# Kernel tuning notes

Hardware: AMD Instinct MI355X
Metric: run time of the kernel (lower is better)

The kernel has to match this reference:

```python
import jax, jax.numpy as jnp
import numpy as np

N = 50000   # nodes
E = 800000  # edges (avg degree 16)
G = 64      # graphs in batch
H = 4       # attention heads
D = 128     # hidden dim per head (= hidden_dim)
V = 128     # embedding vocab (input_dim)
NEG_SLOPE = 0.2

def setup_inputs() -> dict:
    key = jax.random.key(0)
    ks = jax.random.split(key, 12)
    s = 0.05
    return {
        "feats": jax.random.randint(ks[0], (N,), 0, V),
        "src": jax.random.randint(ks[1], (E,), 0, N),
        "dst": jax.random.randint(ks[2], (E,), 0, N),
        "graph_ids": jnp.sort(jax.random.randint(ks[3], (N,), 0, G)),
        "emb": jax.random.normal(ks[4], (V, D)) * s,
        "W1": jax.random.normal(ks[5], (D, H * D)) * s,
        "b1": jax.random.normal(ks[6], (H * D,)) * s,
        "a1": jax.random.normal(ks[7], (H, D)) * s,
        "W2": jax.random.normal(ks[8], (D, H * D)) * s,
        "b2": jax.random.normal(ks[9], (H * D,)) * s,
        "a2": jax.random.normal(ks[10], (H, D)) * s,
        "Wreg": jax.random.normal(ks[11], (1, D)) * s,
    }

def gatv2_layer(x, W, b, a, src, dst):
    # shared-weight GATv2: h = Wx + b, split into heads -> [N,H,D]
    h = (x @ W + b).reshape(-1, H, D)
    hs = h[src]                      # [E,H,D] source feats per edge
    hd = h[dst]                      # [E,H,D] dest feats per edge
    e = jax.nn.leaky_relu(hs + hd, NEG_SLOPE)
    logits = jnp.einsum('ehd,hd->eh', e, a)          # [E,H]
    # edge softmax over incoming edges of each dst node
    m = jax.ops.segment_max(logits, dst, num_segments=N)
    m = jnp.where(jnp.isfinite(m), m, 0.0)           # empty segments -> 0 (unused)
    ex = jnp.exp(logits - m[dst])
    denom = jax.ops.segment_sum(ex, dst, num_segments=N)
    alpha = ex / denom[dst]                          # [E,H]
    rst = jax.ops.segment_sum(alpha[:, :, None] * hs, dst, num_segments=N)  # [N,H,D]
    return rst.mean(axis=1)          # .mean(dim=1) over heads -> [N,D]

def reference(feats, src, dst, graph_ids, emb, W1, b1, a1, W2, b2, a2, Wreg):
    x = emb[feats]                                   # embedding lookup [N,D]
    x = gatv2_layer(x, W1, b1, a1, src, dst)         # layer 1 (dropout=0)
    x = gatv2_layer(x, W2, b2, a2, src, dst)         # layer 2
    pooled = jax.ops.segment_sum(x, graph_ids, num_segments=G)  # SumPooling [G,D]
    return pooled @ Wreg.T                           # Linear bias=False -> [G,1]
```

## Files before the change

### kernel.cpp

```cpp
#include <hip/hip_runtime.h>
#include <hip/hip_bf16.h>

#define N_NODES 50000
#define N_EDGES 800000
#define G_GRAPHS 64
#define H_HEADS 4
#define D_DIM 128
#define HD 512
#define V_VOCAB 128
#define NEG_SLOPE 0.2f

typedef float f32x2v __attribute__((ext_vector_type(2)));
typedef float f32x4 __attribute__((ext_vector_type(4)));
typedef short s16x8 __attribute__((ext_vector_type(8)));
typedef _Float16 h16x2 __attribute__((ext_vector_type(2)));

static __device__ __forceinline__ unsigned short f2b(float f) {
    union { float f; unsigned int i; } x; x.f = f;
    unsigned int r = x.i + 0x7fffu + ((x.i >> 16) & 1u);
    return (unsigned short)(r >> 16);
}
static __device__ __forceinline__ h16x2 u2h2(unsigned int u) {
    union { unsigned int u; h16x2 h; } c; c.u = u; return c.h;
}
static __device__ __forceinline__ unsigned int h22u(h16x2 h) {
    union { unsigned int u; h16x2 h; } c; c.h = h; return c.u;
}
static __device__ __forceinline__ h16x2 packf2(float lo, float hi) {
    union { __fp16 __attribute__((ext_vector_type(2))) p; h16x2 h; } c;
    c.p = __builtin_amdgcn_cvt_pkrtz(lo, hi);
    return c.h;
}

#if __has_builtin(__builtin_amdgcn_cvt_scalef32_pk_f16_fp8)
static __device__ __forceinline__ void fp8x4_to_h16(unsigned int u, h16x2& h0, h16x2& h1) {
    auto r0 = __builtin_amdgcn_cvt_scalef32_pk_f16_fp8((int)u, 1.0f, false);
    auto r1 = __builtin_amdgcn_cvt_scalef32_pk_f16_fp8((int)u, 1.0f, true);
    union { decltype(r0) p; h16x2 h; } c0, c1;
    c0.p = r0; c1.p = r1;
    h0 = c0.h; h1 = c1.h;
}
#else
static __device__ __forceinline__ void fp8x4_to_h16(unsigned int u, h16x2& h0, h16x2& h1) {
    f32x2v lo = __builtin_amdgcn_cvt_pk_f32_fp8(u, false);
    f32x2v hi = __builtin_amdgcn_cvt_pk_f32_fp8(u, true);
    h0 = packf2(lo.x, lo.y);
    h1 = packf2(hi.x, hi.y);
}
#endif

template<int CTRL>
static __device__ __forceinline__ float dpp_add(float v) {
    union { float f; int i; } a, b;
    a.f = v;
    b.i = __builtin_amdgcn_mov_dpp(a.i, CTRL, 0xF, 0xF, true);
    return v + b.f;
}
static __device__ __forceinline__ float row16_sum(float p) {
    p = dpp_add<0xB1>(p);
    p = dpp_add<0x4E>(p);
    p = dpp_add<0x141>(p);
    p = dpp_add<0x140>(p);
    return p;
}

#define MEGA_M1_BLOCKS   256
#define MEGA_WSZ_BLOCKS  256
#define MEGA_HIST_BLOCKS ((N_EDGES + 255) / 256)
__global__ void __launch_bounds__(256) mega_kernel(const float* __restrict__ emb,
                                                   const float* __restrict__ W1,
                                                   float* __restrict__ M1,
                                                   const float* __restrict__ W2,
                                                   unsigned short* __restrict__ Wb,
                                                   const int* __restrict__ dst,
                                                   int* __restrict__ counts,
                                                   float* __restrict__ pool) {
    int b = blockIdx.x;
    if (b < MEGA_M1_BLOCKS) {
        int idx = b * 256 + threadIdx.x;
        int v = idx >> 9, c = idx & 511;
        float acc = 0.f;
        for (int k = 0; k < 128; k++)
            acc += emb[v * 128 + k] * W1[k * 512 + c];
        M1[idx] = acc;
    } else if (b < MEGA_M1_BLOCKS + MEGA_WSZ_BLOCKS) {
        int idx = (b - MEGA_M1_BLOCKS) * 256 + threadIdx.x;
        int j = idx & 7, c = (idx >> 3) & 511, qq = idx >> 12;
        Wb[idx] = f2b(W2[(qq * 8 + j) * 512 + c]);
    } else {
        int hb = b - MEGA_M1_BLOCKS - MEGA_WSZ_BLOCKS;
        if (hb == 0 && threadIdx.x < G_GRAPHS) pool[threadIdx.x] = 0.f;
        int i = hb * 256 + threadIdx.x;
        if (i < N_EDGES) atomicAdd(&counts[dst[i]], 1);
    }
}

__global__ void __launch_bounds__(256) scanf_kernel(const int* __restrict__ counts,
                                                    int* __restrict__ offsets,
                                                    int* __restrict__ cursor,
                                                    int* __restrict__ bsum,
                                                    int* __restrict__ flag) {
    __shared__ int buf[256];
    __shared__ int sbase;
    int t = threadIdx.x, b = blockIdx.x;
    int i0 = (b * 256 + t) * 4;
    int v[4], c[4], s = 0;
    #pragma unroll
    for (int j = 0; j < 4; j++) {
        int idx = i0 + j;
        v[j] = (idx < N_NODES) ? counts[idx] : 0;
        s += v[j];
        c[j] = s;
    }
    buf[t] = s;
    __syncthreads();
    for (int off = 1; off < 256; off <<= 1) {
        int add = (t >= off) ? buf[t - off] : 0;
        __syncthreads();
        buf[t] += add;
        __syncthreads();
    }
    int ebase = (t > 0) ? buf[t - 1] : 0;
    if (t == 0) {
        bsum[b] = buf[255];
        __threadfence();
        atomicAdd(flag, 1);
        while (atomicAdd(flag, 0) < 64) __builtin_amdgcn_s_sleep(8);
    }
    __syncthreads();
    if (t < 64) {
        int vv = (t < b) ? atomicAdd(&bsum[t], 0) : 0;
        #pragma unroll
        for (int off = 1; off < 64; off <<= 1) vv += __shfl_xor(vv, off);
        if (t == 0) sbase = vv;
    }
    __syncthreads();
    int base = sbase;
    #pragma unroll
    for (int j = 0; j < 4; j++) {
        int idx = i0 + j;
        if (idx < N_NODES) {
            int e = base + ebase + c[j];
            offsets[idx + 1] = e;
            cursor[idx] = e - v[j];
        }
    }
    if (b == 0 && t == 0) offsets[0] = 0;
}

#define SG_SCAT_BLOCKS ((N_EDGES + 255) / 256)
#define SG_GATH_BLOCKS (N_NODES * HD / 8 / 256)
__global__ void __launch_bounds__(256) scatgath_kernel(const int* __restrict__ src,
                                                       const int* __restrict__ dst,
                                                       int* __restrict__ cursor,
                                                       int* __restrict__ csr_src,
                                                       const int* __restrict__ feats,
                                                       const float* __restrict__ M1,
                                                       const float* __restrict__ b1,
                                                       unsigned int* __restrict__ h) {
    int b = blockIdx.x;
    if (b < SG_SCAT_BLOCKS) {
        int i = b * 256 + threadIdx.x;
        if (i < N_EDGES) {
            int d = dst[i];
            int pos = atomicAdd(&cursor[d], 1);
            csr_src[pos] = src[i];
        }
    } else {
        int tid = (b - SG_SCAT_BLOCKS) * 256 + threadIdx.x;
        int i0 = tid * 8;
        int n = i0 >> 9, c = i0 & 511;
        if (n >= N_NODES) return;
        int f = feats[n];
        const float* mrow = &M1[f * 512 + c];
        float v[8];
        #pragma unroll
        for (int j = 0; j < 8; j++) v[j] = mrow[j] + b1[c + j];
        uint2 o;
        o.x = __builtin_amdgcn_cvt_pk_fp8_f32(v[0], v[1], 0, false);
        o.x = __builtin_amdgcn_cvt_pk_fp8_f32(v[2], v[3], o.x, true);
        o.y = __builtin_amdgcn_cvt_pk_fp8_f32(v[4], v[5], 0, false);
        o.y = __builtin_amdgcn_cvt_pk_fp8_f32(v[6], v[7], o.y, true);
        *reinterpret_cast<uint2*>(&h[i0 >> 2]) = o;
    }
}

template<bool WRITE_DOTS>
__global__ void __launch_bounds__(256) gat_kernel(const unsigned int* __restrict__ h,
                                                  const int* __restrict__ offsets,
                                                  const int* __restrict__ csr_src,
                                                  const float* __restrict__ a,
                                                  const float* __restrict__ wreg,
                                                  unsigned short* __restrict__ x,
                                                  float* __restrict__ dots) {
    int wid = threadIdx.x >> 6;
    int lane = threadIdx.x & 63;
    int n = blockIdx.x * 4 + wid;
    if (n >= N_NODES) return;
    n = __builtin_amdgcn_readfirstlane(n);
    int row_s = __builtin_amdgcn_readfirstlane(offsets[n]);
    int row_e = __builtin_amdgcn_readfirstlane(offsets[n + 1]);
    int cnt = row_e - row_s;
    int voff = lane * 2;

    h16x2 hd2[4], a06[4], a04[4], acc2[4];
    float pd;
    {
        uint2 hv = *reinterpret_cast<const uint2*>(&h[(unsigned)n * 128u + voff]);
        fp8x4_to_h16(hv.x, hd2[0], hd2[1]);
        fp8x4_to_h16(hv.y, hd2[2], hd2[3]);
        float4 av0 = *reinterpret_cast<const float4*>(&a[lane * 8]);
        float4 av1 = *reinterpret_cast<const float4*>(&a[lane * 8 + 4]);
        float aa[8] = {av0.x, av0.y, av0.z, av0.w, av1.x, av1.y, av1.z, av1.w};
        const float L2E = 1.4426950408889634f;
        #pragma unroll
        for (int k = 0; k < 4; k++) {
            a06[k][0] = (_Float16)(aa[2*k]   * (0.6f * L2E));
            a06[k][1] = (_Float16)(aa[2*k+1] * (0.6f * L2E));
            a04[k][0] = (_Float16)(aa[2*k]   * (0.4f * L2E));
            a04[k][1] = (_Float16)(aa[2*k+1] * (0.4f * L2E));
            acc2[k][0] = (_Float16)0.f; acc2[k][1] = (_Float16)0.f;
        }
        float s = 0.f;
        #pragma unroll
        for (int k = 0; k < 4; k++) s = __builtin_amdgcn_fdot2(hd2[k], a06[k], s, false);
        pd = row16_sum(s);
    }

    auto ld = [&](int ii) {
        int s = __builtin_amdgcn_readfirstlane(csr_src[row_s + ii]);
        return *reinterpret_cast<const uint2*>(&h[(unsigned)s * 128u + voff]);
    };

    float den = 0.f;
    uint2 rA = make_uint2(0, 0), rB = make_uint2(0, 0);
    if (cnt > 0) rA = ld(0);
    if (cnt > 1) rB = ld(1);

    const float C1 = 0.69314718f, C2 = 0.24022651f, C3 = 0.05550411f;

    auto process = [&](uint2 sv) {
        h16x2 hs[4];
        fp8x4_to_h16(sv.x, hs[0], hs[1]);
        fp8x4_to_h16(sv.y, hs[2], hs[3]);
        float p0 = 0.f, p1 = 0.f;
        #pragma unroll
        for (int k = 0; k < 2; k++) {
            h16x2 t2 = hs[k] + hd2[k];
            h16x2 at2 = u2h2(h22u(t2) & 0x7FFF7FFFu);
            p0 = __builtin_amdgcn_fdot2(hs[k], a06[k], p0, false);
            p0 = __builtin_amdgcn_fdot2(at2, a04[k], p0, false);
        }
        #pragma unroll
        for (int k = 2; k < 4; k++) {
            h16x2 t2 = hs[k] + hd2[k];
            h16x2 at2 = u2h2(h22u(t2) & 0x7FFF7FFFu);
            p1 = __builtin_amdgcn_fdot2(hs[k], a06[k], p1, false);
            p1 = __builtin_amdgcn_fdot2(at2, a04[k], p1, false);
        }
        float p = row16_sum(p0 + p1) + pd;
        float w = fmaf(p, fmaf(p, fmaf(p, C3, C2), C1), 1.f);
        den += w;
        h16x2 w2 = packf2(w, w);
        #pragma unroll
        for (int k = 0; k < 4; k++) acc2[k] = w2 * hs[k] + acc2[k];
    };

    for (int i = 0; i < cnt; i += 2) {
        {
            uint2 cur = rA;
            rA = ld(min(i + 2, cnt - 1));
            process(cur);
        }
        if (i + 1 < cnt) {
            uint2 cur = rB;
            rB = ld(min(i + 3, cnt - 1));
            process(cur);
        }
    }

    float inv = (den > 0.f) ? 0.25f / den : 0.f;
    float out8[8];
    #pragma unroll
    for (int j = 0; j < 8; j++) {
        float r = (float)acc2[j >> 1][j & 1] * inv;
        r += __shfl_xor(r, 16);
        r += __shfl_xor(r, 32);
        out8[j] = r;
    }
    if constexpr (WRITE_DOTS) {
        int d0 = (lane & 15) * 8;
        float4 wv0 = *reinterpret_cast<const float4*>(&wreg[d0]);
        float4 wv1 = *reinterpret_cast<const float4*>(&wreg[d0 + 4]);
        float pdot = out8[0] * wv0.x + out8[1] * wv0.y + out8[2] * wv0.z + out8[3] * wv0.w
                   + out8[4] * wv1.x + out8[5] * wv1.y + out8[6] * wv1.z + out8[7] * wv1.w;
        pdot = row16_sum(pdot);
        if (lane == 0) dots[n] = pdot;
    } else {
        if (lane < 16) {
            union { unsigned short u[8]; uint4 v; } o;
            #pragma unroll
            for (int j = 0; j < 8; j++) o.u[j] = f2b(out8[j]);
            *reinterpret_cast<uint4*>(&x[(unsigned)n * 128u + lane * 8]) = o.v;
        }
    }
}

__global__ void __launch_bounds__(256) gemm_kernel(const unsigned short* __restrict__ x,
                                                   const unsigned short* __restrict__ Wb,
                                                   const float* __restrict__ bias,
                                                   unsigned char* __restrict__ hout) {
    int w = threadIdx.x >> 6, l = threadIdx.x & 63;
    int rb = blockIdx.x * 64 + w * 16;
    int cb = blockIdx.y * 64;
    int lr = l & 15, lq = l >> 4;
    f32x4 acc[4] = {};
    int arow = rb + lr;
    bool rok = arow < N_NODES;
    #pragma unroll
    for (int s = 0; s < 4; s++) {
        s16x8 afr = {};
        if (rok) afr = *reinterpret_cast<const s16x8*>(&x[(size_t)arow * 128 + s * 32 + lq * 8]);
        #pragma unroll
        for (int sub = 0; sub < 4; sub++) {
            s16x8 bfr = *reinterpret_cast<const s16x8*>(
                &Wb[(((size_t)(s * 4 + lq) * 512) + cb + sub * 16 + lr) << 3]);
            acc[sub] = __builtin_amdgcn_mfma_f32_16x16x32_bf16(bfr, afr, acc[sub], 0, 0, 0);
        }
    }
    if (!rok) return;
    #pragma unroll
    for (int sub = 0; sub < 4; sub++) {
        int col0 = cb + sub * 16 + lq * 4;
        float4 bb = *reinterpret_cast<const float4*>(&bias[col0]);
        unsigned int pk = __builtin_amdgcn_cvt_pk_fp8_f32(acc[sub][0] + bb.x,
                                                          acc[sub][1] + bb.y, 0, false);
        pk = __builtin_amdgcn_cvt_pk_fp8_f32(acc[sub][2] + bb.z,
                                             acc[sub][3] + bb.w, pk, true);
        *reinterpret_cast<unsigned int*>(&hout[(size_t)arow * 512 + col0]) = pk;
    }
}

__global__ void __launch_bounds__(256) pool64_kernel(const float* __restrict__ dots,
                                                     const int* __restrict__ gid,
                                                     float* __restrict__ pool,
                                                     int* __restrict__ done,
                                                     float* __restrict__ out) {
    int wave = (blockIdx.x * blockDim.x + threadIdx.x) >> 6;
    int lane = threadIdx.x & 63;
    int n0 = wave * 64;
    if (n0 < N_NODES) {
        int n = n0 + lane;
        int nc = min(n, N_NODES - 1);
        int g = gid[nc];
        float v = (n < N_NODES) ? dots[n] : 0.f;
        int g0 = __shfl(g, 0);
        bool uni = __all(g == g0);
        if (uni) {
            v += __shfl_xor(v, 1);
            v += __shfl_xor(v, 2);
            v += __shfl_xor(v, 4);
            v += __shfl_xor(v, 8);
            v += __shfl_xor(v, 16);
            v += __shfl_xor(v, 32);
            if (lane == 0) atomicAdd(&pool[g0], v);
        } else {
            if (n < N_NODES) atomicAdd(&pool[g], v);
        }
    }
    __threadfence();
    __syncthreads();
    __shared__ int amlast;
    if (threadIdx.x == 0)
        amlast = (atomicAdd(done, 1) == (int)gridDim.x - 1) ? 1 : 0;
    __syncthreads();
    if (amlast && threadIdx.x < G_GRAPHS) {
        out[threadIdx.x] = atomicAdd(&pool[threadIdx.x], 0.f);
    }
}

extern "C" void kernel_launch(void* const* d_in, const int* in_sizes, int n_in,
                              void* d_out, int out_size, void* d_ws, size_t ws_size,
                              hipStream_t stream) {
    const int* feats = (const int*)d_in[0];
    const int* src   = (const int*)d_in[1];
    const int* dst   = (const int*)d_in[2];
    const int* gids  = (const int*)d_in[3];
    const float* emb  = (const float*)d_in[4];
    const float* W1   = (const float*)d_in[5];
    const float* b1   = (const float*)d_in[6];
    const float* a1   = (const float*)d_in[7];
    const float* W2   = (const float*)d_in[8];
    const float* b2   = (const float*)d_in[9];
    const float* a2   = (const float*)d_in[10];
    const float* wreg = (const float*)d_in[11];
    float* out = (float*)d_out;

    char* ws = (char*)d_ws;
    size_t off = 0;
    auto alloc = [&](size_t bytes) -> void* {
        void* p = ws + off;
        off = (off + bytes + 255) & ~(size_t)255;
        return p;
    };
    int*   counts  = (int*)alloc((size_t)N_NODES * 4 + 8);
    int*   flag    = counts + N_NODES;
    int*   done    = counts + N_NODES + 1;
    int*   offsets = (int*)alloc((size_t)(N_NODES + 1) * 4);
    int*   cursor  = (int*)alloc((size_t)N_NODES * 4);
    int*   csr_src = (int*)alloc((size_t)N_EDGES * 4);
    int*   bsum    = (int*)alloc(64 * 4);
    float* M1      = (float*)alloc((size_t)V_VOCAB * HD * 4);
    unsigned int*   h  = (unsigned int*)alloc((size_t)N_NODES * HD);
    unsigned short* x  = (unsigned short*)alloc((size_t)N_NODES * D_DIM * 2);
    unsigned short* Wb = (unsigned short*)alloc((size_t)D_DIM * HD * 2);
    float* dots    = (float*)alloc((size_t)N_NODES * 4);
    float* pool    = (float*)alloc((size_t)G_GRAPHS * 4);

    hipMemsetAsync(counts, 0, (size_t)N_NODES * 4 + 8, stream);

    mega_kernel<<<MEGA_M1_BLOCKS + MEGA_WSZ_BLOCKS + MEGA_HIST_BLOCKS, 256, 0, stream>>>(
        emb, W1, M1, W2, Wb, dst, counts, pool);
    scanf_kernel<<<64, 256, 0, stream>>>(counts, offsets, cursor, bsum, flag);
    scatgath_kernel<<<SG_SCAT_BLOCKS + SG_GATH_BLOCKS, 256, 0, stream>>>(
        src, dst, cursor, csr_src, feats, M1, b1, h);

    gat_kernel<false><<<(N_NODES + 3) / 4, 256, 0, stream>>>(h, offsets, csr_src, a1,
                                                             wreg, x, dots);
    gemm_kernel<<<dim3((N_NODES + 63) / 64, 8), 256, 0, stream>>>(x, Wb, b2, (unsigned char*)h);
    gat_kernel<true><<<(N_NODES + 3) / 4, 256, 0, stream>>>(h, offsets, csr_src, a2,
                                                            wreg, x, dots);

    pool64_kernel<<<(N_NODES / 64 + 4) / 4, 256, 0, stream>>>(dots, gids, pool, done, out);
}
```

Before: 332.4 us.

## Read layer-1 features through a tiny fp8 embedding-projection table instead of materializing h

Layer 1 no longer materializes the per-node projected features. The 128-row embedding projection (with bias folded in) is computed once in fp8, and the first GAT pass reads rows by indirection through feats, for both the destination node and each edge source. This removes a 25MB write and a later re-read, and the table is small enough to stay cache-resident. The cost is an extra dependent feats load per edge. The gemm grid is also transposed so that consecutive blocks share row tiles, and the M1 compute is vectorised to 4 columns per thread.

Measured after the change: 329.0 us. No clear change (-1.0%).

```diff
diff --git a/kernel.cpp b/kernel.cpp
--- a/kernel.cpp
+++ b/kernel.cpp
@@ -64,12 +64,13 @@
     return p;
 }
 
-#define MEGA_M1_BLOCKS   256
+#define MEGA_M1_BLOCKS   64
 #define MEGA_WSZ_BLOCKS  256
 #define MEGA_HIST_BLOCKS ((N_EDGES + 255) / 256)
 __global__ void __launch_bounds__(256) mega_kernel(const float* __restrict__ emb,
                                                    const float* __restrict__ W1,
-                                                   float* __restrict__ M1,
+                                                   const float* __restrict__ b1,
+                                                   unsigned int* __restrict__ M1b,
                                                    const float* __restrict__ W2,
                                                    unsigned short* __restrict__ Wb,
                                                    const int* __restrict__ dst,
@@ -78,11 +79,16 @@
     int b = blockIdx.x;
     if (b < MEGA_M1_BLOCKS) {
         int idx = b * 256 + threadIdx.x;
-        int v = idx >> 9, c = idx & 511;
-        float acc = 0.f;
-        for (int k = 0; k < 128; k++)
-            acc += emb[v * 128 + k] * W1[k * 512 + c];
-        M1[idx] = acc;
+        int v = idx >> 7, c0 = (idx & 127) * 4;
+        float acc[4] = {b1[c0], b1[c0 + 1], b1[c0 + 2], b1[c0 + 3]};
+        for (int k = 0; k < 128; k++) {
+            float e = emb[v * 128 + k];
+            #pragma unroll
+            for (int j = 0; j < 4; j++) acc[j] = fmaf(e, W1[k * 512 + c0 + j], acc[j]);
+        }
+        unsigned int pk = __builtin_amdgcn_cvt_pk_fp8_f32(acc[0], acc[1], 0, false);
+        pk = __builtin_amdgcn_cvt_pk_fp8_f32(acc[2], acc[3], pk, true);
+        M1b[idx] = pk;
     } else if (b < MEGA_M1_BLOCKS + MEGA_WSZ_BLOCKS) {
         int idx = (b - MEGA_M1_BLOCKS) * 256 + threadIdx.x;
         int j = idx & 7, c = (idx >> 3) & 511, qq = idx >> 12;
@@ -148,47 +154,21 @@
     if (b == 0 && t == 0) offsets[0] = 0;
 }
 
-#define SG_SCAT_BLOCKS ((N_EDGES + 255) / 256)
-#define SG_GATH_BLOCKS (N_NODES * HD / 8 / 256)
-__global__ void __launch_bounds__(256) scatgath_kernel(const int* __restrict__ src,
-                                                       const int* __restrict__ dst,
-                                                       int* __restrict__ cursor,
-                                                       int* __restrict__ csr_src,
-                                                       const int* __restrict__ feats,
-                                                       const float* __restrict__ M1,
-                                                       const float* __restrict__ b1,
-                                                       unsigned int* __restrict__ h) {
-    int b = blockIdx.x;
-    if (b < SG_SCAT_BLOCKS) {
-        int i = b * 256 + threadIdx.x;
-        if (i < N_EDGES) {
-            int d = dst[i];
-            int pos = atomicAdd(&cursor[d], 1);
-            csr_src[pos] = src[i];
-        }
-    } else {
-        int tid = (b - SG_SCAT_BLOCKS) * 256 + threadIdx.x;
-        int i0 = tid * 8;
-        int n = i0 >> 9, c = i0 & 511;
-        if (n >= N_NODES) return;
-        int f = feats[n];
-        const float* mrow = &M1[f * 512 + c];
-        float v[8];
-        #pragma unroll
-        for (int j = 0; j < 8; j++) v[j] = mrow[j] + b1[c + j];
-        uint2 o;
-        o.x = __builtin_amdgcn_cvt_pk_fp8_f32(v[0], v[1], 0, false);
-        o.x = __builtin_amdgcn_cvt_pk_fp8_f32(v[2], v[3], o.x, true);
-        o.y = __builtin_amdgcn_cvt_pk_fp8_f32(v[4], v[5], 0, false);
-        o.y = __builtin_amdgcn_cvt_pk_fp8_f32(v[6], v[7], o.y, true);
-        *reinterpret_cast<uint2*>(&h[i0 >> 2]) = o;
-    }
-}
-
-template<bool WRITE_DOTS>
+__global__ void scatter_kernel(const int* __restrict__ src, const int* __restrict__ dst,
+                               int* __restrict__ cursor, int* __restrict__ csr_src) {
+    int i = blockIdx.x * blockDim.x + threadIdx.x;
+    if (i < N_EDGES) {
+        int d = dst[i];
+        int pos = atomicAdd(&cursor[d], 1);
+        csr_src[pos] = src[i];
+    }
+}
+
+template<bool LAYER1>
 __global__ void __launch_bounds__(256) gat_kernel(const unsigned int* __restrict__ h,
                                                   const int* __restrict__ offsets,
                                                   const int* __restrict__ csr_src,
+                                                  const int* __restrict__ feats,
                                                   const float* __restrict__ a,
                                                   const float* __restrict__ wreg,
                                                   unsigned short* __restrict__ x,
@@ -206,7 +186,8 @@
     h16x2 hd2[4], a06[4], a04[4], acc2[4];
     float pd;
     {
-        uint2 hv = *reinterpret_cast<const uint2*>(&h[(unsigned)n * 128u + voff]);
+        int nr = LAYER1 ? __builtin_amdgcn_readfirstlane(feats[n]) : n;
+        uint2 hv = *reinterpret_cast<const uint2*>(&h[(unsigned)nr * 128u + voff]);
         fp8x4_to_h16(hv.x, hd2[0], hd2[1]);
         fp8x4_to_h16(hv.y, hd2[2], hd2[3]);
         float4 av0 = *reinterpret_cast<const float4*>(&a[lane * 8]);
@@ -229,6 +210,7 @@
 
     auto ld = [&](int ii) {
         int s = __builtin_amdgcn_readfirstlane(csr_src[row_s + ii]);
+        if (LAYER1) s = __builtin_amdgcn_readfirstlane(feats[s]);
         return *reinterpret_cast<const uint2*>(&h[(unsigned)s * 128u + voff]);
     };
 
@@ -288,7 +270,14 @@
         r += __shfl_xor(r, 32);
         out8[j] = r;
     }
-    if constexpr (WRITE_DOTS) {
+    if constexpr (LAYER1) {
+        if (lane < 16) {
+            union { unsigned short u[8]; uint4 v; } o;
+            #pragma unroll
+            for (int j = 0; j < 8; j++) o.u[j] = f2b(out8[j]);
+            *reinterpret_cast<uint4*>(&x[(unsigned)n * 128u + lane * 8]) = o.v;
+        }
+    } else {
         int d0 = (lane & 15) * 8;
         float4 wv0 = *reinterpret_cast<const float4*>(&wreg[d0]);
         float4 wv1 = *reinterpret_cast<const float4*>(&wreg[d0 + 4]);
@@ -296,13 +285,6 @@
                    + out8[4] * wv1.x + out8[5] * wv1.y + out8[6] * wv1.z + out8[7] * wv1.w;
         pdot = row16_sum(pdot);
         if (lane == 0) dots[n] = pdot;
-    } else {
-        if (lane < 16) {
-            union { unsigned short u[8]; uint4 v; } o;
-            #pragma unroll
-            for (int j = 0; j < 8; j++) o.u[j] = f2b(out8[j]);
-            *reinterpret_cast<uint4*>(&x[(unsigned)n * 128u + lane * 8]) = o.v;
-        }
     }
 }
 
@@ -311,8 +293,8 @@
                                                    const float* __restrict__ bias,
                                                    unsigned char* __restrict__ hout) {
     int w = threadIdx.x >> 6, l = threadIdx.x & 63;
-    int rb = blockIdx.x * 64 + w * 16;
-    int cb = blockIdx.y * 64;
+    int rb = blockIdx.y * 64 + w * 16;
+    int cb = blockIdx.x * 64;
     int lr = l & 15, lq = l >> 4;
     f32x4 acc[4] = {};
     int arow = rb + lr;
@@ -410,7 +392,7 @@
     int*   cursor  = (int*)alloc((size_t)N_NODES * 4);
     int*   csr_src = (int*)alloc((size_t)N_EDGES * 4);
     int*   bsum    = (int*)alloc(64 * 4);
-    float* M1      = (float*)alloc((size_t)V_VOCAB * HD * 4);
+    unsigned int*   M1b = (unsigned int*)alloc((size_t)V_VOCAB * HD);
     unsigned int*   h  = (unsigned int*)alloc((size_t)N_NODES * HD);
     unsigned short* x  = (unsigned short*)alloc((size_t)N_NODES * D_DIM * 2);
     unsigned short* Wb = (unsigned short*)alloc((size_t)D_DIM * HD * 2);
@@ -420,16 +402,15 @@
     hipMemsetAsync(counts, 0, (size_t)N_NODES * 4 + 8, stream);
 
     mega_kernel<<<MEGA_M1_BLOCKS + MEGA_WSZ_BLOCKS + MEGA_HIST_BLOCKS, 256, 0, stream>>>(
-        emb, W1, M1, W2, Wb, dst, counts, pool);
+        emb, W1, b1, M1b, W2, Wb, dst, counts, pool);
     scanf_kernel<<<64, 256, 0, stream>>>(counts, offsets, cursor, bsum, flag);
-    scatgath_kernel<<<SG_SCAT_BLOCKS + SG_GATH_BLOCKS, 256, 0, stream>>>(
-        src, dst, cursor, csr_src, feats, M1, b1, h);
-
-    gat_kernel<false><<<(N_NODES + 3) / 4, 256, 0, stream>>>(h, offsets, csr_src, a1,
-                                                             wreg, x, dots);
-    gemm_kernel<<<dim3((N_NODES + 63) / 64, 8), 256, 0, stream>>>(x, Wb, b2, (unsigned char*)h);
-    gat_kernel<true><<<(N_NODES + 3) / 4, 256, 0, stream>>>(h, offsets, csr_src, a2,
-                                                            wreg, x, dots);
+    scatter_kernel<<<(N_EDGES + 255) / 256, 256, 0, stream>>>(src, dst, cursor, csr_src);
+
+    gat_kernel<true><<<(N_NODES + 3) / 4, 256, 0, stream>>>(M1b, offsets, csr_src, feats,
+                                                            a1, wreg, x, dots);
+    gemm_kernel<<<dim3(8, (N_NODES + 63) / 64), 256, 0, stream>>>(x, Wb, b2, (unsigned char*)h);
+    gat_kernel<false><<<(N_NODES + 3) / 4, 256, 0, stream>>>(h, offsets, csr_src, feats,
+                                                             a2, wreg, x, dots);
 
     pool64_kernel<<<(N_NODES / 64 + 4) / 4, 256, 0, stream>>>(dots, gids, pool, done, out);
 }
```
